# Performance work log

Measured on AMD Instinct MI355X. Metric: run time of the kernel, lower is better.

## Reference

```python
import jax, jax.numpy as jnp
import numpy as np

G = 64          # graphs in batch
NODES = 512     # nodes per graph
CAND = 2048     # edge candidates per graph
D = 256         # in_dim
H = 256         # hid_size
ENS = 2         # ensemble
N = G * NODES   # 32768 total nodes
E = G * CAND    # 131072 total candidate edges


def setup_inputs() -> dict:
    key = jax.random.key(0)
    ks = jax.random.split(key, 8)
    s = lambda fan: 1.0 / np.sqrt(fan)
    node_feat = jax.random.normal(ks[0], (N, D), jnp.float32)
    edge_candidate = jax.random.randint(ks[1], (E, 2), 0, NODES, jnp.int32)
    nnodes = jnp.full((G,), NODES, jnp.int32)
    num_edge_candidate = jnp.full((G,), CAND, jnp.int32)
    W_enc = jax.random.normal(ks[2], (D, D), jnp.float32) * s(D)
    b_enc = jnp.zeros((D,), jnp.float32)
    W1 = jax.random.normal(ks[3], (2 * D, H), jnp.float32) * s(2 * D)
    b1 = jnp.zeros((H,), jnp.float32)
    W2 = jax.random.normal(ks[4], (H, H), jnp.float32) * s(H)
    b2 = jnp.zeros((H,), jnp.float32)
    W3 = jax.random.normal(ks[5], (H, ENS), jnp.float32) * s(H)
    b3 = jnp.zeros((ENS,), jnp.float32)
    return {
        'node_feat': node_feat, 'edge_candidate': edge_candidate,
        'nnodes': nnodes, 'num_edge_candidate': num_edge_candidate,
        'W_enc': W_enc, 'b_enc': b_enc,
        'W1': W1, 'b1': b1, 'W2': W2, 'b2': b2, 'W3': W3, 'b3': b3,
    }


def reference(node_feat, edge_candidate, nnodes, num_edge_candidate,
              W_enc, b_enc, W1, b1, W2, b2, W3, b3):
    # atom encoder (linear stand-in): x [N, D]
    x = node_feat @ W_enc + b_enc
    # per-graph node offsets: [0, cumsum(nnodes)[:-1]]
    edge_rel = jnp.concatenate([jnp.zeros((1,), nnodes.dtype), jnp.cumsum(nnodes)[:-1]])
    offsets = jnp.repeat(edge_rel, num_edge_candidate,
                         total_repeat_length=edge_candidate.shape[0])
    edge_candidate_idx = edge_candidate + offsets[:, None]  # [E, 2] global indices
    # gather endpoint embeddings and concat: [E, 2D]
    h = jnp.concatenate([x[edge_candidate_idx[:, 0]], x[edge_candidate_idx[:, 1]]], axis=-1)
    # MLP: Linear+ReLU, Linear+ReLU, Linear
    h = jax.nn.relu(h @ W1 + b1)
    h = jax.nn.relu(h @ W2 + b2)
    scores = h @ W3 + b3  # [E, ENS]
    return scores, edge_candidate_idx
```

## Files before the change

### kernel.cpp

```cpp
#include <hip/hip_runtime.h>
#include <hip/hip_bf16.h>

typedef short short8 __attribute__((ext_vector_type(8)));
typedef float f32x4 __attribute__((ext_vector_type(4)));

__device__ __forceinline__ ushort f2bf(float f) {
    union { float f; unsigned u; } v; v.f = f;
    unsigned r = v.u + 0x7fff + ((v.u >> 16) & 1);
    return (ushort)(r >> 16);
}

__device__ __forceinline__ void gload_lds16(const void* g, void* l) {
    __builtin_amdgcn_global_load_lds((const __attribute__((address_space(1))) void*)g,
                                     (__attribute__((address_space(3))) void*)l, 16, 0, 0);
}

__global__ __launch_bounds__(256) void prep_k(
    const float* __restrict__ node_feat, ushort* __restrict__ nf_bf, int n4,
    const int* __restrict__ ec, const int* __restrict__ nnodes, const int* __restrict__ ncand,
    int G, int E, int* __restrict__ idxb, float* __restrict__ out_idx,
    const float* __restrict__ W2, ushort* __restrict__ pk2,
    const float* __restrict__ We, const float* __restrict__ be,
    const float* __restrict__ W1, const float* __restrict__ b1,
    ushort* __restrict__ pk1, float* __restrict__ bc)
{
    const int b = blockIdx.x;
    if (b < 2048) {
        int i = b * 256 + threadIdx.x;
        const int stride = 2048 * 256;
        for (int j = i; j < n4; j += stride) {
            float4 v = ((const float4*)node_feat)[j];
            ushort4 o;
            o.x = f2bf(v.x); o.y = f2bf(v.y); o.z = f2bf(v.z); o.w = f2bf(v.w);
            ((ushort4*)nf_bf)[j] = o;
        }
    } else if (b < 2560) {
        __shared__ int snoff[257];
        __shared__ int seoff[257];
        if (threadIdx.x == 0) {
            int a = 0, c = 0;
            for (int g = 0; g < G; g++) {
                snoff[g] = a; a += nnodes[g];
                c += ncand[g]; seoff[g] = c;
            }
        }
        __syncthreads();
        int e = (b - 2048) * 256 + threadIdx.x;
        if (e >= E) return;
        int lo = 0, hi = G - 1;
        while (lo < hi) {
            int mid = (lo + hi) >> 1;
            if (seoff[mid] > e) hi = mid; else lo = mid + 1;
        }
        int off = snoff[lo];
        int g0 = ec[2 * e] + off, g1 = ec[2 * e + 1] + off;
        idxb[2 * e] = g0; idxb[2 * e + 1] = g1;
        out_idx[2 * e] = (float)g0; out_idx[2 * e + 1] = (float)g1;
    } else if (b < 2816) {
        int id = (b - 2560) * 256 + threadIdx.x;
        int j = id & 7;
        int l = (id >> 3) & 63;
        int S = (id >> 9) & 7;
        int F = id >> 12;
        int n = F * 16 + (l & 15);
        int k = S * 32 + (l >> 4) * 8 + j;
        pk2[id] = f2bf(W2[(size_t)k * 256 + n]);
    } else {
        int k = b - 2816;
        int n = threadIdx.x;
        if (k < 512) {
            const float* werow = We + (size_t)(k & 255) * 256;
            const float* w1col = W1 + ((k >> 8) ? 256 * 256 : 0);
            float acc = 0.f;
#pragma unroll 4
            for (int d = 0; d < 256; d++)
                acc += werow[d] * w1col[(size_t)d * 256 + n];
            int j = k & 7;
            int S = k >> 5;
            int F = n >> 4;
            int l = ((k >> 3) & 3) * 16 + (n & 15);
            pk1[((size_t)(F * 16 + S) * 64 + l) * 8 + j] = f2bf(acc);
        } else {
            float acc = b1[n];
#pragma unroll 4
            for (int d = 0; d < 256; d++)
                acc += be[d] * (W1[(size_t)d * 256 + n] + W1[(size_t)(d + 256) * 256 + n]);
            bc[n] = acc;
        }
    }
}


#define LOADB(bk, Bp, KDIV32, t)                                                            \
    _Pragma("unroll") for (int nf = 0; nf < 4; nf++)                                        \
    _Pragma("unroll") for (int kk = 0; kk < 2; kk++)                                        \
        bk[nf * 2 + kk] = *(const short8*)&Bp[((size_t)((wn * 4 + nf) * (KDIV32)            \
                                               + (t) * 2 + kk) * 64 + l) * 8];

#define COMPUTE1(bi, bk)                                                                    \
    _Pragma("unroll") for (int mf = 0; mf < 4; mf++) {                                      \
        short8 af[2];                                                                       \
        _Pragma("unroll") for (int kk = 0; kk < 2; kk++)                                    \
            af[kk] = *(const short8*)&ring[(bi) * 8192 +                                    \
                (wm * 64 + mf * 16 + llo) * 64 + (((kk * 4 + lhi) ^ (llo & 7)) * 8)];       \
        __builtin_amdgcn_s_setprio(1);                                                      \
        _Pragma("unroll") for (int nf = 0; nf < 4; nf++)                                    \
        _Pragma("unroll") for (int kk = 0; kk < 2; kk++)                                    \
            acc[mf][nf] = __builtin_amdgcn_mfma_f32_16x16x32_bf16(                          \
                bk[nf * 2 + kk], af[kk], acc[mf][nf], 0, 0, 0);                             \
        __builtin_amdgcn_s_setprio(0);                                                      \
    }

#define COMPUTE2(t2, bk)                                                                    \
    _Pragma("unroll") for (int mf = 0; mf < 4; mf++) {                                      \
        short8 af[2];                                                                       \
        _Pragma("unroll") for (int kk = 0; kk < 2; kk++)                                    \
            af[kk] = *(const short8*)&h1lds[                                                \
                (wm * 64 + mf * 16 + llo) * 256 +                                           \
                (((t2) * 8 | ((kk * 4 + lhi) ^ (llo & 7))) * 8)];                           \
        __builtin_amdgcn_s_setprio(1);                                                      \
        _Pragma("unroll") for (int nf = 0; nf < 4; nf++)                                    \
        _Pragma("unroll") for (int kk = 0; kk < 2; kk++)                                    \
            acc[mf][nf] = __builtin_amdgcn_mfma_f32_16x16x32_bf16(                          \
                bk[nf * 2 + kk], af[kk], acc[mf][nf], 0, 0, 0);                             \
        __builtin_amdgcn_s_setprio(0);                                                      \
    }

#define TILE_BARRIER(n)                                                                     \
    __builtin_amdgcn_sched_barrier(0);                                                      \
    asm volatile("s_waitcnt vmcnt(" #n ")" ::: "memory");                                   \
    __builtin_amdgcn_s_barrier();                                                           \
    __builtin_amdgcn_sched_barrier(0);

__global__ __launch_bounds__(512, 4) void fused_mlp(
    const ushort* __restrict__ nf_bf, const int* __restrict__ idx,
    const ushort* __restrict__ pk1, const float* __restrict__ bc,
    const ushort* __restrict__ pk2, const float* __restrict__ b2,
    const float* __restrict__ W3, const float* __restrict__ b3,
    float* __restrict__ scores)
{
    __shared__ __align__(16) ushort smem[34816];
    ushort* ring = smem;
    ushort* h1lds = smem;
    float* sc = (float*)&smem[32768];

    const int tid = threadIdx.x;
    const int w = tid >> 6, l = tid & 63;
    const int llo = l & 15, lhi = l >> 4;
    const int wm = w >> 2, wn = w & 3;
    const int work = ((blockIdx.x & 7) << 7) + (blockIdx.x >> 3);
    const int m0 = work * 128;

    const int srow = tid >> 3;
    const int swz = 8 * ((l & 7) ^ (srow & 7));
    const int2 ipa = *(const int2*)&idx[2 * (m0 + srow)];
    const int2 ipb = *(const int2*)&idx[2 * (m0 + srow + 64)];
    const ushort* rp0a = nf_bf + (size_t)ipa.x * 256 + swz;
    const ushort* rp1a = nf_bf + (size_t)ipa.y * 256 + swz;
    const ushort* rp0b = nf_bf + (size_t)ipb.x * 256 + swz;
    const ushort* rp1b = nf_bf + (size_t)ipb.y * 256 + swz;

    f32x4 acc[4][4];
#pragma unroll
    for (int mf = 0; mf < 4; mf++)
#pragma unroll
        for (int nf = 0; nf < 4; nf++) acc[mf][nf] = {0.f, 0.f, 0.f, 0.f};

    short8 bk[8];

    auto stageA = [&](int bi, int t) {
        const int ko = (t & 3) << 6;
        gload_lds16(((t < 4) ? rp0a : rp1a) + ko, &ring[bi * 8192 + srow * 64 + (l & 7) * 8]);
        gload_lds16(((t < 4) ? rp0b : rp1b) + ko, &ring[bi * 8192 + (srow + 64) * 64 + (l & 7) * 8]);
    };

    stageA(0, 0);
    LOADB(bk, pk1, 16, 0)
    stageA(1, 1);
    TILE_BARRIER(10)

#pragma unroll
    for (int t = 0; t < 8; t++) {
        if (t + 2 < 8) stageA((t + 2) % 3, t + 2);
        COMPUTE1(t % 3, bk)
        if (t + 1 < 8) { LOADB(bk, pk1, 16, t + 1) }
        if (t < 6)      { TILE_BARRIER(10) }
        else if (t == 6){ TILE_BARRIER(8) }
    }

    LOADB(bk, pk2, 8, 0)
    __syncthreads();

#pragma unroll
    for (int nf = 0; nf < 4; nf++) {
        int colb = wn * 64 + nf * 16 + lhi * 4;
        float4 bv = *(const float4*)&bc[colb];
        int c = colb >> 3;
        int coff = colb & 7;
#pragma unroll
        for (int mf = 0; mf < 4; mf++) {
            int row = wm * 64 + mf * 16 + llo;
            float v0 = fmaxf(acc[mf][nf][0] + bv.x, 0.f);
            float v1 = fmaxf(acc[mf][nf][1] + bv.y, 0.f);
            float v2 = fmaxf(acc[mf][nf][2] + bv.z, 0.f);
            float v3 = fmaxf(acc[mf][nf][3] + bv.w, 0.f);
            ushort4 o;
            o.x = f2bf(v0); o.y = f2bf(v1); o.z = f2bf(v2); o.w = f2bf(v3);
            int cs = (c & 24) | ((c & 7) ^ (row & 7));
            *(ushort4*)&h1lds[row * 256 + cs * 8 + coff] = o;
        }
    }
    __syncthreads();

#pragma unroll
    for (int mf = 0; mf < 4; mf++)
#pragma unroll
        for (int nf = 0; nf < 4; nf++) acc[mf][nf] = {0.f, 0.f, 0.f, 0.f};

#pragma unroll
    for (int t2 = 0; t2 < 4; t2++) {
        COMPUTE2(t2, bk)
        if (t2 + 1 < 4) { LOADB(bk, pk2, 8, t2 + 1) }
    }

    float p0[4], p1[4];
#pragma unroll
    for (int mf = 0; mf < 4; mf++) { p0[mf] = 0.f; p1[mf] = 0.f; }
#pragma unroll
    for (int nf = 0; nf < 4; nf++) {
        int colb = wn * 64 + nf * 16 + lhi * 4;
        float4 b2v = *(const float4*)&b2[colb];
        float2 w3a = ((const float2*)W3)[colb + 0];
        float2 w3b = ((const float2*)W3)[colb + 1];
        float2 w3c = ((const float2*)W3)[colb + 2];
        float2 w3d = ((const float2*)W3)[colb + 3];
#pragma unroll
        for (int mf = 0; mf < 4; mf++) {
            float v0 = fmaxf(acc[mf][nf][0] + b2v.x, 0.f);
            float v1 = fmaxf(acc[mf][nf][1] + b2v.y, 0.f);
            float v2 = fmaxf(acc[mf][nf][2] + b2v.z, 0.f);
            float v3 = fmaxf(acc[mf][nf][3] + b2v.w, 0.f);
            p0[mf] += v0 * w3a.x + v1 * w3b.x + v2 * w3c.x + v3 * w3d.x;
            p1[mf] += v0 * w3a.y + v1 * w3b.y + v2 * w3c.y + v3 * w3d.y;
        }
    }
#pragma unroll
    for (int mf = 0; mf < 4; mf++) {
        p0[mf] += __shfl_xor(p0[mf], 16); p0[mf] += __shfl_xor(p0[mf], 32);
        p1[mf] += __shfl_xor(p1[mf], 16); p1[mf] += __shfl_xor(p1[mf], 32);
    }
    if (l < 16) {
#pragma unroll
        for (int mf = 0; mf < 4; mf++) {
            int r = wm * 64 + mf * 16 + l;
            sc[(wn * 128 + r) * 2 + 0] = p0[mf];
            sc[(wn * 128 + r) * 2 + 1] = p1[mf];
        }
    }
    __syncthreads();
    if (tid < 256) {
        int row = tid >> 1, j = tid & 1;
        float s = b3[j];
#pragma unroll
        for (int q = 0; q < 4; q++) s += sc[(q * 128 + row) * 2 + j];
        scores[(size_t)(m0 + row) * 2 + j] = s;
    }
}


extern "C" void kernel_launch(void* const* d_in, const int* in_sizes, int n_in,
                              void* d_out, int out_size, void* d_ws, size_t ws_size,
                              hipStream_t stream) {
    const float* node_feat = (const float*)d_in[0];
    const int* edge_candidate = (const int*)d_in[1];
    const int* nnodes = (const int*)d_in[2];
    const int* ncand = (const int*)d_in[3];
    const float* W_enc = (const float*)d_in[4];
    const float* b_enc = (const float*)d_in[5];
    const float* W1 = (const float*)d_in[6];
    const float* b1 = (const float*)d_in[7];
    const float* W2 = (const float*)d_in[8];
    const float* b2 = (const float*)d_in[9];
    const float* W3 = (const float*)d_in[10];
    const float* b3 = (const float*)d_in[11];

    const int D = 256;
    const int G = in_sizes[2];
    const int TOTN = in_sizes[0] / D;
    const int E = in_sizes[1] / 2;
    const int ENS = in_sizes[11];

    char* wsb = (char*)d_ws;
    size_t off = 0;
    auto alloc = [&](size_t bytes) -> void* {
        void* p = wsb + off;
        off += (bytes + 255) & ~(size_t)255;
        return p;
    };
    ushort* nf_bf = (ushort*)alloc((size_t)TOTN * D * 2);
    ushort* pk1   = (ushort*)alloc((size_t)512 * 256 * 2);
    ushort* pk2   = (ushort*)alloc((size_t)256 * 256 * 2);
    float*  bc    = (float*)alloc(256 * 4);
    int* idxb     = (int*)alloc((size_t)E * 2 * 4);

    float* scores_out = (float*)d_out;
    float* idx_out = scores_out + (size_t)E * ENS;

    prep_k<<<3329, 256, 0, stream>>>(
        node_feat, nf_bf, TOTN * D / 4,
        edge_candidate, nnodes, ncand, G, E, idxb, idx_out,
        W2, pk2,
        W_enc, b_enc, W1, b1, pk1, bc);

    fused_mlp<<<E / 128, 512, 0, stream>>>(nf_bf, idxb, pk1, bc, pk2, b2, W3, b3, scores_out);
}
```

Baseline: 81.35 us.

## Fuse fp32-to-bf16 node feature conversion into the gather stage of fused MLP

Drops the separate pass in the prep kernel that converts all node features to bf16, which reads 32 MB and writes 16 MB. The fused MLP now gathers fp32 rows into registers, converts them to bf16 and writes them to swizzled LDS itself, replacing the direct global-to-LDS loads. This removes a full-tensor conversion pass but doubles the gather bytes, since each edge fetches fp32 rows, and the loads now go through registers. That raises register pressure and adds conversion ALU work and LDS store waits inside the pipelined loop.

```diff
diff --git a/kernel.cpp b/kernel.cpp
--- a/kernel.cpp
+++ b/kernel.cpp
@@ -15,8 +15,13 @@
                                      (__attribute__((address_space(3))) void*)l, 16, 0, 0);
 }
 
+__device__ __forceinline__ unsigned pk2bf(float a, float b) {
+    __hip_bfloat162 h = __float22bfloat162_rn(make_float2(a, b));
+    union { __hip_bfloat162 h2; unsigned u; } c; c.h2 = h;
+    return c.u;
+}
+
 __global__ __launch_bounds__(256) void prep_k(
-    const float* __restrict__ node_feat, ushort* __restrict__ nf_bf, int n4,
     const int* __restrict__ ec, const int* __restrict__ nnodes, const int* __restrict__ ncand,
     int G, int E, int* __restrict__ idxb, float* __restrict__ out_idx,
     const float* __restrict__ W2, ushort* __restrict__ pk2,
@@ -25,16 +30,7 @@
     ushort* __restrict__ pk1, float* __restrict__ bc)
 {
     const int b = blockIdx.x;
-    if (b < 2048) {
-        int i = b * 256 + threadIdx.x;
-        const int stride = 2048 * 256;
-        for (int j = i; j < n4; j += stride) {
-            float4 v = ((const float4*)node_feat)[j];
-            ushort4 o;
-            o.x = f2bf(v.x); o.y = f2bf(v.y); o.z = f2bf(v.z); o.w = f2bf(v.w);
-            ((ushort4*)nf_bf)[j] = o;
-        }
-    } else if (b < 2560) {
+    if (b < 512) {
         __shared__ int snoff[257];
         __shared__ int seoff[257];
         if (threadIdx.x == 0) {
@@ -45,7 +41,7 @@
             }
         }
         __syncthreads();
-        int e = (b - 2048) * 256 + threadIdx.x;
+        int e = b * 256 + threadIdx.x;
         if (e >= E) return;
         int lo = 0, hi = G - 1;
         while (lo < hi) {
@@ -56,8 +52,8 @@
         int g0 = ec[2 * e] + off, g1 = ec[2 * e + 1] + off;
         idxb[2 * e] = g0; idxb[2 * e + 1] = g1;
         out_idx[2 * e] = (float)g0; out_idx[2 * e + 1] = (float)g1;
-    } else if (b < 2816) {
-        int id = (b - 2560) * 256 + threadIdx.x;
+    } else if (b < 768) {
+        int id = (b - 512) * 256 + threadIdx.x;
         int j = id & 7;
         int l = (id >> 3) & 63;
         int S = (id >> 9) & 7;
@@ -66,7 +62,7 @@
         int k = S * 32 + (l >> 4) * 8 + j;
         pk2[id] = f2bf(W2[(size_t)k * 256 + n]);
     } else {
-        int k = b - 2816;
+        int k = b - 768;
         int n = threadIdx.x;
         if (k < 512) {
             const float* werow = We + (size_t)(k & 255) * 256;
@@ -126,14 +122,29 @@
         __builtin_amdgcn_s_setprio(0);                                                      \
     }
 
-#define TILE_BARRIER(n)                                                                     \
-    __builtin_amdgcn_sched_barrier(0);                                                      \
-    asm volatile("s_waitcnt vmcnt(" #n ")" ::: "memory");                                   \
-    __builtin_amdgcn_s_barrier();                                                           \
-    __builtin_amdgcn_sched_barrier(0);
+#define ISSUEA(t, s)                                                                        \
+    {                                                                                       \
+        const float* ba = ((t) < 4) ? rpa0 : rpa1;                                          \
+        const float* bb = ((t) < 4) ? rpb0 : rpb1;                                          \
+        const int ko = ((t) & 3) << 6;                                                      \
+        s[0] = *(const float4*)(ba + ko);                                                   \
+        s[1] = *(const float4*)(ba + ko + 4);                                               \
+        s[2] = *(const float4*)(bb + ko);                                                   \
+        s[3] = *(const float4*)(bb + ko + 4);                                               \
+    }
+
+#define WRITEA(t, s)                                                                        \
+    {                                                                                       \
+        ushort* da = &ring[((t) % 3) * 8192 + srow * 64 + cs8];                             \
+        ushort* db = &ring[((t) % 3) * 8192 + (srow + 64) * 64 + cs8];                      \
+        *(uint4*)da = make_uint4(pk2bf(s[0].x, s[0].y), pk2bf(s[0].z, s[0].w),              \
+                                 pk2bf(s[1].x, s[1].y), pk2bf(s[1].z, s[1].w));             \
+        *(uint4*)db = make_uint4(pk2bf(s[2].x, s[2].y), pk2bf(s[2].z, s[2].w),              \
+                                 pk2bf(s[3].x, s[3].y), pk2bf(s[3].z, s[3].w));             \
+    }
 
 __global__ __launch_bounds__(512, 4) void fused_mlp(
-    const ushort* __restrict__ nf_bf, const int* __restrict__ idx,
+    const float* __restrict__ nf, const int* __restrict__ idx,
     const ushort* __restrict__ pk1, const float* __restrict__ bc,
     const ushort* __restrict__ pk2, const float* __restrict__ b2,
     const float* __restrict__ W3, const float* __restrict__ b3,
@@ -152,62 +163,72 @@
     const int m0 = work * 128;
 
     const int srow = tid >> 3;
-    const int swz = 8 * ((l & 7) ^ (srow & 7));
+    const int cs8 = 8 * ((l & 7) ^ (srow & 7));
+    const int ksub = (l & 7) * 8;
     const int2 ipa = *(const int2*)&idx[2 * (m0 + srow)];
     const int2 ipb = *(const int2*)&idx[2 * (m0 + srow + 64)];
-    const ushort* rp0a = nf_bf + (size_t)ipa.x * 256 + swz;
-    const ushort* rp1a = nf_bf + (size_t)ipa.y * 256 + swz;
-    const ushort* rp0b = nf_bf + (size_t)ipb.x * 256 + swz;
-    const ushort* rp1b = nf_bf + (size_t)ipb.y * 256 + swz;
+    const float* rpa0 = nf + (size_t)ipa.x * 256 + ksub;
+    const float* rpa1 = nf + (size_t)ipa.y * 256 + ksub;
+    const float* rpb0 = nf + (size_t)ipb.x * 256 + ksub;
+    const float* rpb1 = nf + (size_t)ipb.y * 256 + ksub;
 
     f32x4 acc[4][4];
 #pragma unroll
     for (int mf = 0; mf < 4; mf++)
 #pragma unroll
-        for (int nf = 0; nf < 4; nf++) acc[mf][nf] = {0.f, 0.f, 0.f, 0.f};
+        for (int nf2 = 0; nf2 < 4; nf2++) acc[mf][nf2] = {0.f, 0.f, 0.f, 0.f};
 
     short8 bk[8];
-
-    auto stageA = [&](int bi, int t) {
-        const int ko = (t & 3) << 6;
-        gload_lds16(((t < 4) ? rp0a : rp1a) + ko, &ring[bi * 8192 + srow * 64 + (l & 7) * 8]);
-        gload_lds16(((t < 4) ? rp0b : rp1b) + ko, &ring[bi * 8192 + (srow + 64) * 64 + (l & 7) * 8]);
-    };
-
-    stageA(0, 0);
+    float4 s0[4], s1[4];
+
+    ISSUEA(0, s0)
+    ISSUEA(1, s1)
     LOADB(bk, pk1, 16, 0)
-    stageA(1, 1);
-    TILE_BARRIER(10)
+    __builtin_amdgcn_sched_barrier(0);
+    asm volatile("s_waitcnt vmcnt(12)" ::: "memory");
+    __builtin_amdgcn_sched_barrier(0);
+    WRITEA(0, s0)
+    asm volatile("s_waitcnt lgkmcnt(0)" ::: "memory");
+    __builtin_amdgcn_s_barrier();
+    __builtin_amdgcn_sched_barrier(0);
 
 #pragma unroll
     for (int t = 0; t < 8; t++) {
-        if (t + 2 < 8) stageA((t + 2) % 3, t + 2);
         COMPUTE1(t % 3, bk)
         if (t + 1 < 8) { LOADB(bk, pk1, 16, t + 1) }
-        if (t < 6)      { TILE_BARRIER(10) }
-        else if (t == 6){ TILE_BARRIER(8) }
+        if (t + 2 < 8) { if (t & 1) ISSUEA(t + 2, s1) else ISSUEA(t + 2, s0) }
+        if (t + 1 < 8) {
+            __builtin_amdgcn_sched_barrier(0);
+            if (t + 2 < 8) { asm volatile("s_waitcnt vmcnt(12)" ::: "memory"); }
+            else           { asm volatile("s_waitcnt vmcnt(8)"  ::: "memory"); }
+            __builtin_amdgcn_sched_barrier(0);
+            if (t & 1) WRITEA(t + 1, s0) else WRITEA(t + 1, s1)
+            asm volatile("s_waitcnt lgkmcnt(0)" ::: "memory");
+            __builtin_amdgcn_s_barrier();
+            __builtin_amdgcn_sched_barrier(0);
+        }
     }
 
     LOADB(bk, pk2, 8, 0)
     __syncthreads();
 
 #pragma unroll
-    for (int nf = 0; nf < 4; nf++) {
-        int colb = wn * 64 + nf * 16 + lhi * 4;
+    for (int nf2 = 0; nf2 < 4; nf2++) {
+        int colb = wn * 64 + nf2 * 16 + lhi * 4;
         float4 bv = *(const float4*)&bc[colb];
         int c = colb >> 3;
         int coff = colb & 7;
 #pragma unroll
         for (int mf = 0; mf < 4; mf++) {
             int row = wm * 64 + mf * 16 + llo;
-            float v0 = fmaxf(acc[mf][nf][0] + bv.x, 0.f);
-            float v1 = fmaxf(acc[mf][nf][1] + bv.y, 0.f);
-            float v2 = fmaxf(acc[mf][nf][2] + bv.z, 0.f);
-            float v3 = fmaxf(acc[mf][nf][3] + bv.w, 0.f);
+            float v0 = fmaxf(acc[mf][nf2][0] + bv.x, 0.f);
+            float v1 = fmaxf(acc[mf][nf2][1] + bv.y, 0.f);
+            float v2 = fmaxf(acc[mf][nf2][2] + bv.z, 0.f);
+            float v3 = fmaxf(acc[mf][nf2][3] + bv.w, 0.f);
             ushort4 o;
             o.x = f2bf(v0); o.y = f2bf(v1); o.z = f2bf(v2); o.w = f2bf(v3);
-            int cs = (c & 24) | ((c & 7) ^ (row & 7));
-            *(ushort4*)&h1lds[row * 256 + cs * 8 + coff] = o;
+            int cw = (c & 24) | ((c & 7) ^ (row & 7));
+            *(ushort4*)&h1lds[row * 256 + cw * 8 + coff] = o;
         }
     }
     __syncthreads();
@@ -215,7 +236,7 @@
 #pragma unroll
     for (int mf = 0; mf < 4; mf++)
 #pragma unroll
-        for (int nf = 0; nf < 4; nf++) acc[mf][nf] = {0.f, 0.f, 0.f, 0.f};
+        for (int nf2 = 0; nf2 < 4; nf2++) acc[mf][nf2] = {0.f, 0.f, 0.f, 0.f};
 
 #pragma unroll
     for (int t2 = 0; t2 < 4; t2++) {
@@ -227,8 +248,8 @@
 #pragma unroll
     for (int mf = 0; mf < 4; mf++) { p0[mf] = 0.f; p1[mf] = 0.f; }
 #pragma unroll
-    for (int nf = 0; nf < 4; nf++) {
-        int colb = wn * 64 + nf * 16 + lhi * 4;
+    for (int nf2 = 0; nf2 < 4; nf2++) {
+        int colb = wn * 64 + nf2 * 16 + lhi * 4;
         float4 b2v = *(const float4*)&b2[colb];
         float2 w3a = ((const float2*)W3)[colb + 0];
         float2 w3b = ((const float2*)W3)[colb + 1];
@@ -236,10 +257,10 @@
         float2 w3d = ((const float2*)W3)[colb + 3];
 #pragma unroll
         for (int mf = 0; mf < 4; mf++) {
-            float v0 = fmaxf(acc[mf][nf][0] + b2v.x, 0.f);
-            float v1 = fmaxf(acc[mf][nf][1] + b2v.y, 0.f);
-            float v2 = fmaxf(acc[mf][nf][2] + b2v.z, 0.f);
-            float v3 = fmaxf(acc[mf][nf][3] + b2v.w, 0.f);
+            float v0 = fmaxf(acc[mf][nf2][0] + b2v.x, 0.f);
+            float v1 = fmaxf(acc[mf][nf2][1] + b2v.y, 0.f);
+            float v2 = fmaxf(acc[mf][nf2][2] + b2v.z, 0.f);
+            float v3 = fmaxf(acc[mf][nf2][3] + b2v.w, 0.f);
             p0[mf] += v0 * w3a.x + v1 * w3b.x + v2 * w3c.x + v3 * w3d.x;
             p1[mf] += v0 * w3a.y + v1 * w3b.y + v2 * w3c.y + v3 * w3d.y;
         }
@@ -284,9 +305,7 @@
     const float* W3 = (const float*)d_in[10];
     const float* b3 = (const float*)d_in[11];
 
-    const int D = 256;
     const int G = in_sizes[2];
-    const int TOTN = in_sizes[0] / D;
     const int E = in_sizes[1] / 2;
     const int ENS = in_sizes[11];
 
@@ -297,20 +316,18 @@
         off += (bytes + 255) & ~(size_t)255;
         return p;
     };
-    ushort* nf_bf = (ushort*)alloc((size_t)TOTN * D * 2);
-    ushort* pk1   = (ushort*)alloc((size_t)512 * 256 * 2);
-    ushort* pk2   = (ushort*)alloc((size_t)256 * 256 * 2);
-    float*  bc    = (float*)alloc(256 * 4);
-    int* idxb     = (int*)alloc((size_t)E * 2 * 4);
+    ushort* pk1 = (ushort*)alloc((size_t)512 * 256 * 2);
+    ushort* pk2 = (ushort*)alloc((size_t)256 * 256 * 2);
+    float*  bc  = (float*)alloc(256 * 4);
+    int* idxb   = (int*)alloc((size_t)E * 2 * 4);
 
     float* scores_out = (float*)d_out;
     float* idx_out = scores_out + (size_t)E * ENS;
 
-    prep_k<<<3329, 256, 0, stream>>>(
-        node_feat, nf_bf, TOTN * D / 4,
+    prep_k<<<1281, 256, 0, stream>>>(
         edge_candidate, nnodes, ncand, G, E, idxb, idx_out,
         W2, pk2,
         W_enc, b_enc, W1, b1, pk1, bc);
 
-    fused_mlp<<<E / 128, 512, 0, stream>>>(nf_bf, idxb, pk1, bc, pk2, b2, W3, b3, scores_out);
-}
+    fused_mlp<<<E / 128, 512, 0, stream>>>(node_feat, idxb, pk1, bc, pk2, b2, W3, b3, scores_out);
+}
```

New measurement: 139.7 us. 71.7% more time.

## Precompute per-node first-layer projections and gather them per edge

Applied to the files above, without the earlier changes.

Splits the first MLP layer by linearity: a new node-level GEMM computes the two halves of the first layer (encoder folded in) for every node, storing a bf16 UV buffer. The edge kernel then gathers u[src] and v[dst], adds bias, applies ReLU and feeds layer two, removing the per-edge K=512 GEMM. This cuts first-layer matmul work by roughly the edge-to-node ratio, at the cost of an extra launch, a large intermediate buffer write/read, and extra bf16 rounding of the partial sums.

```diff
diff --git a/kernel.cpp b/kernel.cpp
--- a/kernel.cpp
+++ b/kernel.cpp
@@ -8,6 +8,16 @@
     union { float f; unsigned u; } v; v.f = f;
     unsigned r = v.u + 0x7fff + ((v.u >> 16) & 1);
     return (ushort)(r >> 16);
+}
+
+__device__ __forceinline__ float bf2f(ushort u) {
+    union { unsigned u; float f; } v; v.u = (unsigned)u << 16; return v.f;
+}
+
+__device__ __forceinline__ unsigned pk2bf(float a, float b) {
+    __hip_bfloat162 h = __float22bfloat162_rn(make_float2(a, b));
+    union { __hip_bfloat162 h2; unsigned u; } c; c.h2 = h;
+    return c.u;
 }
 
 __device__ __forceinline__ void gload_lds16(const void* g, void* l) {
@@ -22,7 +32,7 @@
     const float* __restrict__ W2, ushort* __restrict__ pk2,
     const float* __restrict__ We, const float* __restrict__ be,
     const float* __restrict__ W1, const float* __restrict__ b1,
-    ushort* __restrict__ pk1, float* __restrict__ bc)
+    ushort* __restrict__ pkA, float* __restrict__ bc)
 {
     const int b = blockIdx.x;
     if (b < 2048) {
@@ -65,28 +75,29 @@
         int n = F * 16 + (l & 15);
         int k = S * 32 + (l >> 4) * 8 + j;
         pk2[id] = f2bf(W2[(size_t)k * 256 + n]);
+    } else if (b < 3328) {
+        int id = b - 2816;
+        int k = id >> 1;
+        int n = (id & 1) * 256 + threadIdx.x;
+        const float* werow = We + (size_t)k * 256;
+        const float* w1col = W1 + ((n >> 8) ? 256 * 256 : 0);
+        int h = n & 255;
+        float acc = 0.f;
+#pragma unroll 4
+        for (int d = 0; d < 256; d++)
+            acc += werow[d] * w1col[(size_t)d * 256 + h];
+        int F = n >> 4;
+        int S = k >> 5;
+        int j = k & 7;
+        int l = ((k >> 3) & 3) * 16 + (n & 15);
+        pkA[((size_t)(F * 8 + S) * 64 + l) * 8 + j] = f2bf(acc);
     } else {
-        int k = b - 2816;
         int n = threadIdx.x;
-        if (k < 512) {
-            const float* werow = We + (size_t)(k & 255) * 256;
-            const float* w1col = W1 + ((k >> 8) ? 256 * 256 : 0);
-            float acc = 0.f;
+        float acc = b1[n];
 #pragma unroll 4
-            for (int d = 0; d < 256; d++)
-                acc += werow[d] * w1col[(size_t)d * 256 + n];
-            int j = k & 7;
-            int S = k >> 5;
-            int F = n >> 4;
-            int l = ((k >> 3) & 3) * 16 + (n & 15);
-            pk1[((size_t)(F * 16 + S) * 64 + l) * 8 + j] = f2bf(acc);
-        } else {
-            float acc = b1[n];
-#pragma unroll 4
-            for (int d = 0; d < 256; d++)
-                acc += be[d] * (W1[(size_t)d * 256 + n] + W1[(size_t)(d + 256) * 256 + n]);
-            bc[n] = acc;
-        }
+        for (int d = 0; d < 256; d++)
+            acc += be[d] * (W1[(size_t)d * 256 + n] + W1[(size_t)(d + 256) * 256 + n]);
+        bc[n] = acc;
     }
 }
 
@@ -132,15 +143,75 @@
     __builtin_amdgcn_s_barrier();                                                           \
     __builtin_amdgcn_sched_barrier(0);
 
-__global__ __launch_bounds__(512, 4) void fused_mlp(
-    const ushort* __restrict__ nf_bf, const int* __restrict__ idx,
-    const ushort* __restrict__ pk1, const float* __restrict__ bc,
-    const ushort* __restrict__ pk2, const float* __restrict__ b2,
-    const float* __restrict__ W3, const float* __restrict__ b3,
-    float* __restrict__ scores)
+__global__ __launch_bounds__(512, 4) void uv_gemm(
+    const ushort* __restrict__ nf_bf, const ushort* __restrict__ pkA,
+    ushort* __restrict__ uv)
+{
+    __shared__ __align__(16) ushort ring[3 * 8192];
+
+    const int tid = threadIdx.x;
+    const int w = tid >> 6, l = tid & 63;
+    const int llo = l & 15, lhi = l >> 4;
+    const int wm = w >> 2, wn = w & 3;
+    const int work = ((blockIdx.x & 7) << 6) + (blockIdx.x >> 3);
+    const int mt = work >> 1, nh = work & 1;
+    const int m0 = mt * 128;
+
+    const int srow = tid >> 3;
+    const int swz = 8 * ((l & 7) ^ (srow & 7));
+    const ushort* rpa = nf_bf + (size_t)(m0 + srow) * 256 + swz;
+    const ushort* rpb = nf_bf + (size_t)(m0 + srow + 64) * 256 + swz;
+    const ushort* Bp = pkA + (size_t)nh * 65536;
+
+    f32x4 acc[4][4];
+#pragma unroll
+    for (int mf = 0; mf < 4; mf++)
+#pragma unroll
+        for (int nf2 = 0; nf2 < 4; nf2++) acc[mf][nf2] = {0.f, 0.f, 0.f, 0.f};
+
+    short8 bk[8];
+
+    auto stageA = [&](int bi, int t) {
+        gload_lds16(rpa + t * 64, &ring[bi * 8192 + srow * 64 + (l & 7) * 8]);
+        gload_lds16(rpb + t * 64, &ring[bi * 8192 + (srow + 64) * 64 + (l & 7) * 8]);
+    };
+
+    stageA(0, 0);
+    LOADB(bk, Bp, 8, 0)
+    stageA(1, 1);
+    TILE_BARRIER(10)
+
+#pragma unroll
+    for (int t = 0; t < 4; t++) {
+        if (t + 2 < 4) stageA((t + 2) % 3, t + 2);
+        COMPUTE1(t % 3, bk)
+        if (t + 1 < 4) { LOADB(bk, Bp, 8, t + 1) }
+        if (t == 0)      { TILE_BARRIER(10) }
+        else if (t == 1) { TILE_BARRIER(10) }
+        else if (t == 2) { TILE_BARRIER(8) }
+    }
+
+#pragma unroll
+    for (int mf = 0; mf < 4; mf++) {
+        int row = m0 + wm * 64 + mf * 16 + llo;
+#pragma unroll
+        for (int nf2 = 0; nf2 < 4; nf2++) {
+            int col = nh * 256 + wn * 64 + nf2 * 16 + lhi * 4;
+            ushort4 o;
+            o.x = f2bf(acc[mf][nf2][0]); o.y = f2bf(acc[mf][nf2][1]);
+            o.z = f2bf(acc[mf][nf2][2]); o.w = f2bf(acc[mf][nf2][3]);
+            *(ushort4*)&uv[(size_t)row * 512 + col] = o;
+        }
+    }
+}
+
+__global__ __launch_bounds__(512, 4) void edge_mlp(
+    const ushort* __restrict__ uv, const int* __restrict__ idx,
+    const float* __restrict__ bc, const ushort* __restrict__ pk2,
+    const float* __restrict__ b2, const float* __restrict__ W3,
+    const float* __restrict__ b3, float* __restrict__ scores)
 {
     __shared__ __align__(16) ushort smem[34816];
-    ushort* ring = smem;
     ushort* h1lds = smem;
     float* sc = (float*)&smem[32768];
 
@@ -151,71 +222,41 @@
     const int work = ((blockIdx.x & 7) << 7) + (blockIdx.x >> 3);
     const int m0 = work * 128;
 
-    const int srow = tid >> 3;
-    const int swz = 8 * ((l & 7) ^ (srow & 7));
-    const int2 ipa = *(const int2*)&idx[2 * (m0 + srow)];
-    const int2 ipb = *(const int2*)&idx[2 * (m0 + srow + 64)];
-    const ushort* rp0a = nf_bf + (size_t)ipa.x * 256 + swz;
-    const ushort* rp1a = nf_bf + (size_t)ipa.y * 256 + swz;
-    const ushort* rp0b = nf_bf + (size_t)ipb.x * 256 + swz;
-    const ushort* rp1b = nf_bf + (size_t)ipb.y * 256 + swz;
+    {
+        int r = tid >> 2, p = tid & 3;
+        int2 ip = *(const int2*)&idx[2 * (m0 + r)];
+        const ushort* ur = uv + (size_t)ip.x * 512;
+        const ushort* vr = uv + (size_t)ip.y * 512 + 256;
+#pragma unroll
+        for (int cc = 0; cc < 8; cc++) {
+            int c = p * 8 + cc;
+            short8 u8 = *(const short8*)&ur[c * 8];
+            short8 v8 = *(const short8*)&vr[c * 8];
+            float4 ba = *(const float4*)&bc[c * 8];
+            float4 bb = *(const float4*)&bc[c * 8 + 4];
+            float f0 = fmaxf(bf2f((ushort)u8[0]) + bf2f((ushort)v8[0]) + ba.x, 0.f);
+            float f1 = fmaxf(bf2f((ushort)u8[1]) + bf2f((ushort)v8[1]) + ba.y, 0.f);
+            float f2 = fmaxf(bf2f((ushort)u8[2]) + bf2f((ushort)v8[2]) + ba.z, 0.f);
+            float f3 = fmaxf(bf2f((ushort)u8[3]) + bf2f((ushort)v8[3]) + ba.w, 0.f);
+            float f4 = fmaxf(bf2f((ushort)u8[4]) + bf2f((ushort)v8[4]) + bb.x, 0.f);
+            float f5 = fmaxf(bf2f((ushort)u8[5]) + bf2f((ushort)v8[5]) + bb.y, 0.f);
+            float f6 = fmaxf(bf2f((ushort)u8[6]) + bf2f((ushort)v8[6]) + bb.z, 0.f);
+            float f7 = fmaxf(bf2f((ushort)u8[7]) + bf2f((ushort)v8[7]) + bb.w, 0.f);
+            uint4 o = make_uint4(pk2bf(f0, f1), pk2bf(f2, f3), pk2bf(f4, f5), pk2bf(f6, f7));
+            int cw = (c & 24) | ((c & 7) ^ (r & 7));
+            *(uint4*)&h1lds[r * 256 + cw * 8] = o;
+        }
+    }
 
     f32x4 acc[4][4];
 #pragma unroll
     for (int mf = 0; mf < 4; mf++)
 #pragma unroll
-        for (int nf = 0; nf < 4; nf++) acc[mf][nf] = {0.f, 0.f, 0.f, 0.f};
+        for (int nf2 = 0; nf2 < 4; nf2++) acc[mf][nf2] = {0.f, 0.f, 0.f, 0.f};
 
     short8 bk[8];
-
-    auto stageA = [&](int bi, int t) {
-        const int ko = (t & 3) << 6;
-        gload_lds16(((t < 4) ? rp0a : rp1a) + ko, &ring[bi * 8192 + srow * 64 + (l & 7) * 8]);
-        gload_lds16(((t < 4) ? rp0b : rp1b) + ko, &ring[bi * 8192 + (srow + 64) * 64 + (l & 7) * 8]);
-    };
-
-    stageA(0, 0);
-    LOADB(bk, pk1, 16, 0)
-    stageA(1, 1);
-    TILE_BARRIER(10)
-
-#pragma unroll
-    for (int t = 0; t < 8; t++) {
-        if (t + 2 < 8) stageA((t + 2) % 3, t + 2);
-        COMPUTE1(t % 3, bk)
-        if (t + 1 < 8) { LOADB(bk, pk1, 16, t + 1) }
-        if (t < 6)      { TILE_BARRIER(10) }
-        else if (t == 6){ TILE_BARRIER(8) }
-    }
-
     LOADB(bk, pk2, 8, 0)
     __syncthreads();
-
-#pragma unroll
-    for (int nf = 0; nf < 4; nf++) {
-        int colb = wn * 64 + nf * 16 + lhi * 4;
-        float4 bv = *(const float4*)&bc[colb];
-        int c = colb >> 3;
-        int coff = colb & 7;
-#pragma unroll
-        for (int mf = 0; mf < 4; mf++) {
-            int row = wm * 64 + mf * 16 + llo;
-            float v0 = fmaxf(acc[mf][nf][0] + bv.x, 0.f);
-            float v1 = fmaxf(acc[mf][nf][1] + bv.y, 0.f);
-            float v2 = fmaxf(acc[mf][nf][2] + bv.z, 0.f);
-            float v3 = fmaxf(acc[mf][nf][3] + bv.w, 0.f);
-            ushort4 o;
-            o.x = f2bf(v0); o.y = f2bf(v1); o.z = f2bf(v2); o.w = f2bf(v3);
-            int cs = (c & 24) | ((c & 7) ^ (row & 7));
-            *(ushort4*)&h1lds[row * 256 + cs * 8 + coff] = o;
-        }
-    }
-    __syncthreads();
-
-#pragma unroll
-    for (int mf = 0; mf < 4; mf++)
-#pragma unroll
-        for (int nf = 0; nf < 4; nf++) acc[mf][nf] = {0.f, 0.f, 0.f, 0.f};
 
 #pragma unroll
     for (int t2 = 0; t2 < 4; t2++) {
@@ -227,8 +268,8 @@
 #pragma unroll
     for (int mf = 0; mf < 4; mf++) { p0[mf] = 0.f; p1[mf] = 0.f; }
 #pragma unroll
-    for (int nf = 0; nf < 4; nf++) {
-        int colb = wn * 64 + nf * 16 + lhi * 4;
+    for (int nf2 = 0; nf2 < 4; nf2++) {
+        int colb = wn * 64 + nf2 * 16 + lhi * 4;
         float4 b2v = *(const float4*)&b2[colb];
         float2 w3a = ((const float2*)W3)[colb + 0];
         float2 w3b = ((const float2*)W3)[colb + 1];
@@ -236,10 +277,10 @@
         float2 w3d = ((const float2*)W3)[colb + 3];
 #pragma unroll
         for (int mf = 0; mf < 4; mf++) {
-            float v0 = fmaxf(acc[mf][nf][0] + b2v.x, 0.f);
-            float v1 = fmaxf(acc[mf][nf][1] + b2v.y, 0.f);
-            float v2 = fmaxf(acc[mf][nf][2] + b2v.z, 0.f);
-            float v3 = fmaxf(acc[mf][nf][3] + b2v.w, 0.f);
+            float v0 = fmaxf(acc[mf][nf2][0] + b2v.x, 0.f);
+            float v1 = fmaxf(acc[mf][nf2][1] + b2v.y, 0.f);
+            float v2 = fmaxf(acc[mf][nf2][2] + b2v.z, 0.f);
+            float v3 = fmaxf(acc[mf][nf2][3] + b2v.w, 0.f);
             p0[mf] += v0 * w3a.x + v1 * w3b.x + v2 * w3c.x + v3 * w3d.x;
             p1[mf] += v0 * w3a.y + v1 * w3b.y + v2 * w3c.y + v3 * w3d.y;
         }
@@ -298,7 +339,8 @@
         return p;
     };
     ushort* nf_bf = (ushort*)alloc((size_t)TOTN * D * 2);
-    ushort* pk1   = (ushort*)alloc((size_t)512 * 256 * 2);
+    ushort* uv    = (ushort*)alloc((size_t)TOTN * 512 * 2);
+    ushort* pkA   = (ushort*)alloc((size_t)256 * 512 * 2);
     ushort* pk2   = (ushort*)alloc((size_t)256 * 256 * 2);
     float*  bc    = (float*)alloc(256 * 4);
     int* idxb     = (int*)alloc((size_t)E * 2 * 4);
@@ -310,7 +352,9 @@
         node_feat, nf_bf, TOTN * D / 4,
         edge_candidate, nnodes, ncand, G, E, idxb, idx_out,
         W2, pk2,
-        W_enc, b_enc, W1, b1, pk1, bc);
-
-    fused_mlp<<<E / 128, 512, 0, stream>>>(nf_bf, idxb, pk1, bc, pk2, b2, W3, b3, scores_out);
-}
+        W_enc, b_enc, W1, b1, pkA, bc);
+
+    uv_gemm<<<TOTN / 128 * 2, 512, 0, stream>>>(nf_bf, pkA, uv);
+
+    edge_mlp<<<E / 128, 512, 0, stream>>>(uv, idxb, bc, pk2, b2, W3, b3, scores_out);
+}
```

Result: slower. 104.6 us (+28.6%).
